# Kernel tuning notes

Hardware: AMD Instinct MI355X
Metric: run time of the kernel (lower is better)

Reference implementation:

```python
import math
import jax, jax.numpy as jnp
import numpy as np

L, B, N, D, H, DFF = 4, 64, 511, 256, 8, 512
S = N + 1          # +1 game token
HD = D // H
BW = 7             # BOARD_WIDTH (undefined global in source; board-game policy width)


def layer_norm(x, g, b):
    m = jnp.mean(x, axis=-1, keepdims=True)
    v = jnp.var(x, axis=-1, keepdims=True)
    return (x - m) / jnp.sqrt(v + 1e-5) * g + b


def setup_inputs() -> dict:
    key = jax.random.key(0)
    ks = jax.random.split(key, 24)

    def p(k, shape):
        return jax.random.normal(k, shape, jnp.float32) * 0.02

    return {
        "cell_states": jax.random.randint(ks[0], (B * N,), 0, 3, dtype=jnp.int32),
        "edge_type_matrix": jax.random.randint(ks[1], (B, N, N), 0, 3, dtype=jnp.int32),
        "patch_emb": p(ks[2], (3, D)),
        "game_token": p(ks[3], (1, 1, D)),
        "edge_emb": p(ks[4], (3, H)),   # zeros in source init; random here to exercise bias path
        "in_w": p(ks[5], (L, 3 * D, D)), "in_b": p(ks[6], (L, 3 * D)),
        "out_w": p(ks[7], (L, D, D)), "out_b": p(ks[8], (L, D)),
        "ff1_w": p(ks[9], (L, DFF, D)), "ff1_b": p(ks[10], (L, DFF)),
        "ff2_w": p(ks[11], (L, D, DFF)), "ff2_b": p(ks[12], (L, D)),
        "ln1_g": jnp.ones((L, D)), "ln1_b": jnp.zeros((L, D)),
        "ln2_g": jnp.ones((L, D)), "ln2_b": jnp.zeros((L, D)),
        "fc1_w": p(ks[13], (64, D)), "fc1_b": p(ks[14], (64,)),
        "pol_w": p(ks[15], (BW, 64)), "pol_b": p(ks[16], (BW,)),
        "val_w": p(ks[17], (1, 64)), "val_b": p(ks[18], (1,)),
    }


def reference(cell_states, edge_type_matrix, patch_emb, game_token, edge_emb,
              in_w, in_b, out_w, out_b, ff1_w, ff1_b, ff2_w, ff2_b,
              ln1_g, ln1_b, ln2_g, ln2_b, fc1_w, fc1_b, pol_w, pol_b, val_w, val_b):
    # embed cells and prepend game token -> [B, S, D]
    x = patch_emb[cell_states].reshape(B, N, D)
    x = jnp.concatenate([jnp.broadcast_to(game_token, (B, 1, D)), x], axis=1)

    # edge bias: [B,N,N,H] -> [B,H,N,N], pad token row/col with zeros -> [B,H,S,S]
    bias = jnp.transpose(edge_emb[edge_type_matrix], (0, 3, 1, 2))
    bias = jnp.pad(bias, ((0, 0), (0, 0), (1, 0), (1, 0)))

    scale = math.sqrt(HD)
    for i in range(L):
        h = layer_norm(x, ln1_g[i], ln1_b[i])
        qkv = h @ in_w[i].T + in_b[i]                       # [B,S,3D]
        q, k, v = jnp.split(qkv, 3, axis=-1)
        q = q.reshape(B, S, H, HD).transpose(0, 2, 1, 3)    # [B,H,S,HD]
        k = k.reshape(B, S, H, HD).transpose(0, 2, 1, 3)
        v = v.reshape(B, S, H, HD).transpose(0, 2, 1, 3)
        scores = jnp.einsum('bhqd,bhkd->bhqk', q, k) / scale + bias
        attn = jax.nn.softmax(scores, axis=-1)              # dropout = identity (eval)
        o = jnp.einsum('bhqk,bhkd->bhqd', attn, v)
        o = o.transpose(0, 2, 1, 3).reshape(B, S, D)
        x = x + (o @ out_w[i].T + out_b[i])
        h2 = layer_norm(x, ln2_g[i], ln2_b[i])
        x = x + (jax.nn.relu(h2 @ ff1_w[i].T + ff1_b[i]) @ ff2_w[i].T + ff2_b[i])

    g = x[:, 0, :]
    o = jax.nn.relu(g @ fc1_w.T + fc1_b)
    policy_logits = o @ pol_w.T + pol_b
    value = jnp.tanh(o @ val_w.T + val_b)
    return policy_logits, value
```

## Files before the change

### kernel.cpp

```cpp
#include <hip/hip_runtime.h>
#include <hip/hip_bf16.h>
#include <math.h>

#define L_ 4
#define B_ 64
#define N_ 511
#define D_ 256
#define H_ 8
#define DFF_ 512
#define S_ 512
#define HD_ 32
#define BW_ 7
#define BS_ (B_*S_)

typedef __attribute__((ext_vector_type(8))) short short8;
typedef __attribute__((ext_vector_type(4))) short short4v;
typedef __attribute__((ext_vector_type(4))) float f32x4;

#define L2E 1.44269504088896340f
#define QSCL (0.17677669529663687f * 1.44269504088896340f)

#if defined(__HIP_DEVICE_COMPILE__)
#if __has_builtin(__builtin_amdgcn_mfma_f32_16x16x16bf16_1k)
#define MFMA16(p, v, c) __builtin_amdgcn_mfma_f32_16x16x16bf16_1k(p, v, c, 0, 0, 0)
#elif __has_builtin(__builtin_amdgcn_mfma_f32_16x16x16_bf16)
#define MFMA16(p, v, c) __builtin_amdgcn_mfma_f32_16x16x16_bf16(p, v, c, 0, 0, 0)
#else
#define MFMA16(p, v, c) (c)
#endif
#else
#define MFMA16(p, v, c) (c)
#endif

#if defined(__HIP_DEVICE_COMPILE__) && __has_builtin(__builtin_amdgcn_exp2f)
#define EXP2(x) __builtin_amdgcn_exp2f(x)
#else
#define EXP2(x) exp2f(x)
#endif

__device__ inline ushort f2b(float f) {
    unsigned u = __float_as_uint(f);
    unsigned r = (u + 0x7fffu + ((u >> 16) & 1u)) >> 16;
    return (ushort)r;
}

#if defined(__HIP_DEVICE_COMPILE__) && __has_builtin(__builtin_amdgcn_cvt_pk_bf16_f32)
typedef __attribute__((ext_vector_type(2))) __bf16 bf16x2_t;
__device__ inline uint pk_bf16(float a, float b) {
    bf16x2_t r = __builtin_amdgcn_cvt_pk_bf16_f32(a, b);
    return *(uint*)&r;
}
#else
__device__ inline uint pk_bf16(float a, float b) {
    return (uint)f2b(a) | ((uint)f2b(b) << 16);
}
#endif

__device__ inline void bsel4(uint E, uint tlo, uint thi,
                             float b0, float b1, float b2, float bl[4]) {
#if defined(__HIP_DEVICE_COMPILE__) && __has_builtin(__builtin_amdgcn_perm)
    uint E2  = E + E;
    uint E2b = E2 | 0x01010101u;
    uint s01 = __builtin_amdgcn_perm(E2b, E2, 0x05010400u);
    uint s23 = __builtin_amdgcn_perm(E2b, E2, 0x07030602u);
    uint p01 = __builtin_amdgcn_perm(thi, tlo, s01);
    uint p23 = __builtin_amdgcn_perm(thi, tlo, s23);
    bl[0] = __uint_as_float(p01 << 16);
    bl[1] = __uint_as_float(p01 & 0xFFFF0000u);
    bl[2] = __uint_as_float(p23 << 16);
    bl[3] = __uint_as_float(p23 & 0xFFFF0000u);
#else
    #pragma unroll
    for (int i = 0; i < 4; i++) {
        unsigned char e = (unsigned char)((E >> (8 * i)) & 0xff);
        bl[i] = e == 0 ? b0 : (e == 1 ? b1 : (e == 2 ? b2 : 0.f));
    }
#endif
}

__device__ inline void gload16(const void* g, void* l) {
#if __has_builtin(__builtin_amdgcn_global_load_lds)
    __builtin_amdgcn_global_load_lds(
        (const __attribute__((address_space(1))) void*)g,
        (__attribute__((address_space(3))) void*)l, 16, 0, 0);
#else
    *(short8*)l = *(const short8*)g;
#endif
}

__global__ __launch_bounds__(256) void build_x(const int* __restrict__ cs,
                                               const float* __restrict__ patch,
                                               const float* __restrict__ game,
                                               float* __restrict__ x)
{
    int idx = blockIdx.x * 256 + threadIdx.x;
    int row = idx / (D_ / 4);
    int c4  = idx % (D_ / 4);
    int s = row & (S_ - 1);
    float4 v;
    if (s == 0) {
        v = ((const float4*)game)[c4];
    } else {
        int b = row / S_;
        int cell = cs[b * N_ + s - 1];
        v = ((const float4*)(patch + cell * D_))[c4];
    }
    ((float4*)x)[idx] = v;
}

__global__ __launch_bounds__(256) void build_et8(const int* __restrict__ et,
                                                 unsigned char* __restrict__ et8)
{
    long idx = (long)blockIdx.x * 256 + threadIdx.x;
    int k = (int)(idx & (S_ - 1));
    long rem = idx >> 9;
    int q = (int)(rem & (S_ - 1));
    int b = (int)(rem >> 9);
    unsigned char v = 3;
    if (q > 0 && k > 0) {
        v = (unsigned char)et[((long)b * N_ + (q - 1)) * N_ + (k - 1)];
    }
    et8[idx] = v;
}

__global__ __launch_bounds__(256) void convert_f2b(const float* __restrict__ in,
                                                   ushort* __restrict__ out, int n4)
{
    int i = blockIdx.x * 256 + threadIdx.x;
    if (i >= n4) return;
    float4 v = ((const float4*)in)[i];
    ushort4 o4;
    o4.x = f2b(v.x); o4.y = f2b(v.y); o4.z = f2b(v.z); o4.w = f2b(v.w);
    ((ushort4*)out)[i] = o4;
}

__global__ __launch_bounds__(256) void convert_inw(const float* __restrict__ in,
                                                   ushort* __restrict__ out)
{
    int i = blockIdx.x * 256 + threadIdx.x;
    if (i >= 196608) return;
    float4 v = ((const float4*)in)[i];
    int r = (i >> 6) % 768;
    float s = (r < 256) ? (float)QSCL : 1.f;
    ushort4 o4;
    o4.x = f2b(v.x * s); o4.y = f2b(v.y * s); o4.z = f2b(v.z * s); o4.w = f2b(v.w * s);
    ((ushort4*)out)[i] = o4;
}

__global__ __launch_bounds__(256) void ln_kernel(const float* __restrict__ in,
                                                 ushort* __restrict__ out,
                                                 const float* __restrict__ gw,
                                                 const float* __restrict__ bw)
{
    int t = threadIdx.x;
    int lane = t & 63;
    int r = t >> 6;
    size_t row = (size_t)blockIdx.x * 4 + r;
    float4 v = *(const float4*)(in + row * D_ + lane * 4);
    float s = v.x + v.y + v.z + v.w;
    #pragma unroll
    for (int o = 32; o >= 1; o >>= 1) s += __shfl_xor(s, o);
    float mean = s * (1.f / 256.f);
    float dx = v.x - mean, dy = v.y - mean, dz = v.z - mean, dw = v.w - mean;
    float s2 = dx * dx + dy * dy + dz * dz + dw * dw;
    #pragma unroll
    for (int o = 32; o >= 1; o >>= 1) s2 += __shfl_xor(s2, o);
    float rstd = rsqrtf(s2 * (1.f / 256.f) + 1e-5f);
    float4 g  = *(const float4*)(gw + lane * 4);
    float4 bb = *(const float4*)(bw + lane * 4);
    ushort4 o4;
    o4.x = f2b(dx * rstd * g.x + bb.x);
    o4.y = f2b(dy * rstd * g.y + bb.y);
    o4.z = f2b(dz * rstd * g.z + bb.z);
    o4.w = f2b(dw * rstd * g.w + bb.w);
    *(ushort4*)(out + row * D_ + lane * 4) = o4;
}

template<int K, int NT, bool RELU, bool QSC, bool QKV>
__global__ __launch_bounds__(256, 2) void gemm_lds(const ushort* __restrict__ A,
                                                   const ushort* __restrict__ W,
                                                   const float* __restrict__ bias,
                                                   ushort* __restrict__ Cout,
                                                   ushort* __restrict__ Kb,
                                                   ushort* __restrict__ Vt)
{
    __shared__ ushort As[4096];
    __shared__ ushort Ws[4096];
    const int N = NT * 128;
    int t = threadIdx.x;
    int wave = t >> 6, lane = t & 63;
    int lr = lane & 15, quad = lane >> 4;
    int lk = quad * 8;
    int blk = blockIdx.x;
    int xcd = blk & 7, idx = blk >> 3;
    int m0 = (xcd * 32 + (idx & 31)) * 128;
    int n0 = (idx >> 5) * 128;
    int mh = (wave >> 1) * 64, nh = (wave & 1) * 64;

    const ushort* ga0 = A + (size_t)(m0 + (t >> 2)) * K + (t & 3) * 8;
    const ushort* ga1 = ga0 + (size_t)64 * K;
    const ushort* gw0 = W + (size_t)(n0 + (t >> 2)) * K + (t & 3) * 8;
    const ushort* gw1 = gw0 + (size_t)64 * K;
    ushort* la0 = As + t * 8;
    ushort* la1 = As + t * 8 + 2048;
    ushort* lw0 = Ws + t * 8;
    ushort* lw1 = Ws + t * 8 + 2048;

    f32x4 acc[4][4];
    f32x4 zz = {0.f, 0.f, 0.f, 0.f};
    #pragma unroll
    for (int i = 0; i < 4; i++)
        #pragma unroll
        for (int j = 0; j < 4; j++) acc[i][j] = zz;

    for (int k0 = 0; k0 < K; k0 += 32) {
        gload16(ga0 + k0, la0);
        gload16(ga1 + k0, la1);
        gload16(gw0 + k0, lw0);
        gload16(gw1 + k0, lw1);
        __syncthreads();
        short8 af[4], wf[4];
        #pragma unroll
        for (int i = 0; i < 4; i++) af[i] = *(const short8*)&As[(mh + i * 16 + lr) * 32 + lk];
        #pragma unroll
        for (int j = 0; j < 4; j++) wf[j] = *(const short8*)&Ws[(nh + j * 16 + lr) * 32 + lk];
        #pragma unroll
        for (int i = 0; i < 4; i++)
            #pragma unroll
            for (int j = 0; j < 4; j++)
                acc[i][j] = __builtin_amdgcn_mfma_f32_16x16x32_bf16(af[i], wf[j], acc[i][j], 0, 0, 0);
        __syncthreads();
    }

    #pragma unroll
    for (int nt = 0; nt < 4; nt++) {
        int colbase = n0 + nh + nt * 16;
        int col = colbase + lr;
        float bv = bias[col];
        if (QSC && colbase < 256) bv *= (float)QSCL;
        int region = QKV ? (colbase >> 8) : 0;
        #pragma unroll
        for (int mt = 0; mt < 4; mt++) {
            int rowb = m0 + mh + mt * 16 + quad * 4;
            if (!QKV || region == 0) {
                #pragma unroll
                for (int r = 0; r < 4; r++) {
                    size_t cidx = (size_t)(rowb + r) * N + col;
                    float v = acc[mt][nt][r] + bv;
                    if (RELU) v = fmaxf(v, 0.f);
                    Cout[cidx] = f2b(v);
                }
            } else if (region == 1) {
                int hh = (col >> 5) & 7, d = col & 31;
                int bb = rowb >> 9, s = rowb & 511;
                size_t kbase = ((size_t)(bb * 8 + hh) * 512 + s) * 32 + d;
                #pragma unroll
                for (int r = 0; r < 4; r++)
                    Kb[kbase + (size_t)r * 32] = f2b(acc[mt][nt][r] + bv);
            } else {
                int hh = (col >> 5) & 7, d = col & 31;
                int bb = rowb >> 9, s = rowb & 511;
                ushort4 w;
                w.x = f2b(acc[mt][nt][0] + bv);
                w.y = f2b(acc[mt][nt][1] + bv);
                w.z = f2b(acc[mt][nt][2] + bv);
                w.w = f2b(acc[mt][nt][3] + bv);
                size_t vidx = (((size_t)(bb * 8 + hh) * 32 + (s >> 4)) * 32 + d) * 16 + (s & 15);
                *(ushort4*)&Vt[vidx] = w;
            }
        }
    }
}

template<int K>
__global__ __launch_bounds__(256, 2) void gemm_ln(const ushort* __restrict__ A,
                                                  const ushort* __restrict__ W,
                                                  const float* __restrict__ bias,
                                                  float* __restrict__ X,
                                                  const float* __restrict__ lng,
                                                  const float* __restrict__ lnb,
                                                  ushort* __restrict__ Hout)
{
    __shared__ ushort As[64 * 32];
    __shared__ ushort Ws[256 * 32];
    __shared__ float lds_s[64][4];
    __shared__ float lds_q[64][4];
    int t = threadIdx.x;
    int wave = t >> 6, lane = t & 63;
    int lr = lane & 15, quad = lane >> 4;
    int lk = quad * 8;
    int blk = blockIdx.x;
    int xcd = blk & 7;
    int m0 = (xcd * 64 + (blk >> 3)) * 64;
    int nh = wave * 64;

    const ushort* ga = A + (size_t)(m0 + (t >> 2)) * K + (t & 3) * 8;
    const ushort* gw = W + (size_t)(t >> 2) * K + (t & 3) * 8;
    ushort* la = As + t * 8;
    ushort* lw = Ws + t * 8;

    f32x4 acc[4][4];
    f32x4 zz = {0.f, 0.f, 0.f, 0.f};
    #pragma unroll
    for (int i = 0; i < 4; i++)
        #pragma unroll
        for (int j = 0; j < 4; j++) acc[i][j] = zz;

    for (int k0 = 0; k0 < K; k0 += 32) {
        gload16(ga + k0, la);
        #pragma unroll
        for (int j = 0; j < 4; j++)
            gload16(gw + (size_t)(j * 64) * K + k0, lw + j * 2048);
        __syncthreads();
        short8 af[4], wf[4];
        #pragma unroll
        for (int i = 0; i < 4; i++) af[i] = *(const short8*)&As[(i * 16 + lr) * 32 + lk];
        #pragma unroll
        for (int j = 0; j < 4; j++) wf[j] = *(const short8*)&Ws[(nh + j * 16 + lr) * 32 + lk];
        #pragma unroll
        for (int i = 0; i < 4; i++)
            #pragma unroll
            for (int j = 0; j < 4; j++)
                acc[i][j] = __builtin_amdgcn_mfma_f32_16x16x32_bf16(af[i], wf[j], acc[i][j], 0, 0, 0);
        __syncthreads();
    }

    float gc[4], bc[4], bi[4];
    #pragma unroll
    for (int nt = 0; nt < 4; nt++) {
        int col = nh + nt * 16 + lr;
        gc[nt] = lng[col]; bc[nt] = lnb[col]; bi[nt] = bias[col];
    }
    float psum[16], psq[16];
    #pragma unroll
    for (int e = 0; e < 16; e++) { psum[e] = 0.f; psq[e] = 0.f; }
    #pragma unroll
    for (int nt = 0; nt < 4; nt++) {
        #pragma unroll
        for (int mt = 0; mt < 4; mt++) {
            #pragma unroll
            for (int r = 0; r < 4; r++) {
                int row = m0 + mt * 16 + quad * 4 + r;
                size_t idx = (size_t)row * D_ + nh + nt * 16 + lr;
                float v = acc[mt][nt][r] + bi[nt] + X[idx];
                X[idx] = v;
                acc[mt][nt][r] = v;
                psum[mt * 4 + r] += v;
                psq[mt * 4 + r]  += v * v;
            }
        }
    }
    #pragma unroll
    for (int e = 0; e < 16; e++) {
        float s = psum[e], q = psq[e];
        s += __shfl_xor(s, 1); q += __shfl_xor(q, 1);
        s += __shfl_xor(s, 2); q += __shfl_xor(q, 2);
        s += __shfl_xor(s, 4); q += __shfl_xor(q, 4);
        s += __shfl_xor(s, 8); q += __shfl_xor(q, 8);
        psum[e] = s; psq[e] = q;
    }
    if (lr == 0) {
        #pragma unroll
        for (int mt = 0; mt < 4; mt++)
            #pragma unroll
            for (int r = 0; r < 4; r++) {
                int rl = mt * 16 + quad * 4 + r;
                lds_s[rl][wave] = psum[mt * 4 + r];
                lds_q[rl][wave] = psq[mt * 4 + r];
            }
    }
    __syncthreads();
    #pragma unroll
    for (int mt = 0; mt < 4; mt++) {
        #pragma unroll
        for (int r = 0; r < 4; r++) {
            int rl = mt * 16 + quad * 4 + r;
            f32x4 ss = *(const f32x4*)lds_s[rl];
            f32x4 qq = *(const f32x4*)lds_q[rl];
            float s = ss[0] + ss[1] + ss[2] + ss[3];
            float q = qq[0] + qq[1] + qq[2] + qq[3];
            float mean = s * (1.f / 256.f);
            float rstd = rsqrtf(q * (1.f / 256.f) - mean * mean + 1e-5f);
            int row = m0 + mt * 16 + quad * 4 + r;
            #pragma unroll
            for (int nt = 0; nt < 4; nt++) {
                size_t idx = (size_t)row * D_ + nh + nt * 16 + lr;
                float hv = (acc[mt][nt][r] - mean) * rstd * gc[nt] + bc[nt];
                Hout[idx] = f2b(hv);
            }
        }
    }
}

__global__ __launch_bounds__(256, 4) void attn_mfma(const ushort* __restrict__ qkv,
                                                    const ushort* __restrict__ Kb,
                                                    const ushort* __restrict__ Vt,
                                                    const unsigned char* __restrict__ et8,
                                                    const float* __restrict__ eemb,
                                                    ushort* __restrict__ o)
{
    __shared__ unsigned char Est[2][2][4096];
    int t = threadIdx.x;
    int wave = t >> 6, lane = t & 63;
    int lr = lane & 15, quad = lane >> 4;
    int lk = quad * 8;
    int blk = blockIdx.x;
    int b = ((blk >> 7) << 3) | (blk & 7);
    int rest = (blk >> 3) & 15;
    int h = rest & 7;
    int qhalf = rest >> 3;
    int bh = b * 8 + h;
    int q0 = qhalf * 256 + wave * 64;
    float eb0 = eemb[h] * L2E, eb1 = eemb[8 + h] * L2E, eb2 = eemb[16 + h] * L2E;
    uint tlo = (uint)f2b(eb0) | ((uint)f2b(eb1) << 16);
    uint thi = (uint)f2b(eb2);

    short8 qf[4];
    #pragma unroll
    for (int X = 0; X < 4; X++)
        qf[X] = *(const short8*)(qkv + ((size_t)(b * S_ + q0 + X * 16 + lr)) * 768 + h * 32 + lk);
    const ushort* Kp = Kb + ((size_t)(bh * S_ + lr)) * 32 + lk;
    const ushort* Vp = Vt + (size_t)bh * 32 * 512 + lr * 16 + quad * 4;
    const unsigned char* Ep = et8 + ((size_t)(b * S_ + qhalf * 256 + t)) * S_;
    unsigned char* ElD = &Est[0][0][t * 16];

    f32x4 zz = {0.f, 0.f, 0.f, 0.f};
    f32x4 oacc[4][2];
    float lsum[4];
    #pragma unroll
    for (int X = 0; X < 4; X++) { oacc[X][0] = zz; oacc[X][1] = zz; lsum[X] = 0.f; }

    gload16(Ep + 0,  ElD);
    gload16(Ep + 16, ElD + 4096);
    short8 kf0 = *(const short8*)(Kp);
    short8 kf1 = *(const short8*)(Kp + 16 * 32);
    __syncthreads();

    for (int k0 = 0; k0 < S_; k0 += 32) {
        int cb = (k0 >> 5) & 1, nb = cb ^ 1;
        if (k0 < S_ - 32) {
            gload16(Ep + k0 + 32, ElD + (size_t)nb * 8192);
            gload16(Ep + k0 + 48, ElD + (size_t)nb * 8192 + 4096);
        }
        int kn = (k0 + 32) & (S_ - 1);
        short8 nk0 = *(const short8*)(Kp + (size_t)kn * 32);
        short8 nk1 = *(const short8*)(Kp + (size_t)(kn + 16) * 32);
        const ushort* vt0 = Vp + (size_t)(k0 >> 4) * 512;
        short4v vf00 = *(const short4v*)(vt0);
        short4v vf01 = *(const short4v*)(vt0 + 256);
        short4v vf10 = *(const short4v*)(vt0 + 512);
        short4v vf11 = *(const short4v*)(vt0 + 768);
        #pragma unroll
        for (int X = 0; X < 4; X++) {
            f32x4 s0 = __builtin_amdgcn_mfma_f32_16x16x32_bf16(kf0, qf[X], zz, 0, 0, 0);
            f32x4 s1 = __builtin_amdgcn_mfma_f32_16x16x32_bf16(kf1, qf[X], zz, 0, 0, 0);
            int qrow = wave * 64 + X * 16 + lr;
            uint E0 = *(const uint*)&Est[cb][0][qrow * 16 + quad * 4];
            uint E1 = *(const uint*)&Est[cb][1][qrow * 16 + quad * 4];
            float bl0[4], bl1[4];
            bsel4(E0, tlo, thi, eb0, eb1, eb2, bl0);
            bsel4(E1, tlo, thi, eb0, eb1, eb2, bl1);
            float p0[4], p1[4];
            #pragma unroll
            for (int r = 0; r < 4; r++) {
                p0[r] = EXP2(s0[r] + bl0[r]);
                p1[r] = EXP2(s1[r] + bl1[r]);
                lsum[X] += p0[r] + p1[r];
            }
            union { short4v v; uint2 u; } P0, P1;
            P0.u.x = pk_bf16(p0[0], p0[1]); P0.u.y = pk_bf16(p0[2], p0[3]);
            P1.u.x = pk_bf16(p1[0], p1[1]); P1.u.y = pk_bf16(p1[2], p1[3]);
            oacc[X][0] = MFMA16(P0.v, vf00, oacc[X][0]);
            oacc[X][1] = MFMA16(P0.v, vf01, oacc[X][1]);
            oacc[X][0] = MFMA16(P1.v, vf10, oacc[X][0]);
            oacc[X][1] = MFMA16(P1.v, vf11, oacc[X][1]);
        }
        kf0 = nk0; kf1 = nk1;
        __syncthreads();
    }

    #pragma unroll
    for (int X = 0; X < 4; X++) {
        float ls = lsum[X];
        ls += __shfl_xor(ls, 16);
        ls += __shfl_xor(ls, 32);
        #pragma unroll
        for (int r = 0; r < 4; r++) {
            int q = quad * 4 + r;
            float inv = 1.f / __shfl(ls, q);
            size_t base = (size_t)(b * S_ + q0 + X * 16 + q) * D_ + h * 32;
            o[base + lr]      = f2b(oacc[X][0][r] * inv);
            o[base + 16 + lr] = f2b(oacc[X][1][r] * inv);
        }
    }
}

__global__ __launch_bounds__(64) void head_kernel(const float* __restrict__ x,
                                                  const float* __restrict__ fc1w,
                                                  const float* __restrict__ fc1b,
                                                  const float* __restrict__ polw,
                                                  const float* __restrict__ polb,
                                                  const float* __restrict__ valw,
                                                  const float* __restrict__ valb,
                                                  float* __restrict__ out)
{
    __shared__ float o1[64];
    int b = blockIdx.x;
    int t = threadIdx.x;
    const float* g = x + (size_t)b * S_ * D_;
    float acc = fc1b[t];
    for (int k = 0; k < D_; k++) acc += g[k] * fc1w[t * D_ + k];
    o1[t] = fmaxf(acc, 0.f);
    __syncthreads();
    if (t < BW_) {
        float a = polb[t];
        for (int k = 0; k < 64; k++) a += o1[k] * polw[t * 64 + k];
        out[b * BW_ + t] = a;
    } else if (t == BW_) {
        float a = valb[0];
        for (int k = 0; k < 64; k++) a += o1[k] * valw[k];
        out[B_ * BW_ + b] = tanhf(a);
    }
}

extern "C" void kernel_launch(void* const* d_in, const int* in_sizes, int n_in,
                              void* d_out, int out_size, void* d_ws, size_t ws_size,
                              hipStream_t stream)
{
    const int*   cs    = (const int*)d_in[0];
    const int*   etm   = (const int*)d_in[1];
    const float* patch = (const float*)d_in[2];
    const float* game  = (const float*)d_in[3];
    const float* eemb  = (const float*)d_in[4];
    const float* in_w  = (const float*)d_in[5];
    const float* in_b  = (const float*)d_in[6];
    const float* out_w = (const float*)d_in[7];
    const float* out_b = (const float*)d_in[8];
    const float* ff1_w = (const float*)d_in[9];
    const float* ff1_b = (const float*)d_in[10];
    const float* ff2_w = (const float*)d_in[11];
    const float* ff2_b = (const float*)d_in[12];
    const float* ln1_g = (const float*)d_in[13];
    const float* ln1_b = (const float*)d_in[14];
    const float* ln2_g = (const float*)d_in[15];
    const float* ln2_b = (const float*)d_in[16];
    const float* fc1_w = (const float*)d_in[17];
    const float* fc1_b = (const float*)d_in[18];
    const float* pol_w = (const float*)d_in[19];
    const float* pol_b = (const float*)d_in[20];
    const float* val_w = (const float*)d_in[21];
    const float* val_b = (const float*)d_in[22];
    float* out = (float*)d_out;

    char* base = (char*)d_ws;
    float*  x     = (float*)(base + 0);
    ushort* h     = (ushort*)(base + 33554432);
    ushort* qkvb  = (ushort*)(base + 50331648);
    ushort* Kb    = (ushort*)(base + 100663296);
    ushort* Vt    = (ushort*)(base + 117440512);
    ushort* ob    = (ushort*)(base + 134217728);
    unsigned char* et8 = (unsigned char*)(base + 150994944);
    ushort* inwb  = (ushort*)(base + 167772160);
    ushort* outwb = (ushort*)(base + 169345024);
    ushort* ff1wb = (ushort*)(base + 169869312);
    ushort* ff2wb = (ushort*)(base + 170917888);

    build_x<<<8192, 256, 0, stream>>>(cs, patch, game, x);
    build_et8<<<65536, 256, 0, stream>>>(etm, et8);
    convert_inw<<<768, 256, 0, stream>>>(in_w, inwb);
    convert_f2b<<<256, 256, 0, stream>>>(out_w, outwb, 65536);
    convert_f2b<<<512, 256, 0, stream>>>(ff1_w, ff1wb, 131072);
    convert_f2b<<<512, 256, 0, stream>>>(ff2_w, ff2wb, 131072);

    ln_kernel<<<8192, 256, 0, stream>>>(x, h, ln1_g, ln1_b);

    for (int i = 0; i < L_; i++) {
        gemm_lds<256, 6, false, true, true><<<1536, 256, 0, stream>>>(
            h, inwb + (size_t)i * 196608, in_b + i * 768, qkvb, Kb, Vt);
        attn_mfma<<<1024, 256, 0, stream>>>(qkvb, Kb, Vt, et8, eemb, ob);
        gemm_ln<256><<<512, 256, 0, stream>>>(
            ob, outwb + (size_t)i * 65536, out_b + i * 256, x,
            ln2_g + i * D_, ln2_b + i * D_, h);
        gemm_lds<256, 4, true, false, false><<<1024, 256, 0, stream>>>(
            h, ff1wb + (size_t)i * 131072, ff1_b + i * 512, qkvb, nullptr, nullptr);
        int nx = (i + 1 < L_) ? (i + 1) : i;
        gemm_ln<512><<<512, 256, 0, stream>>>(
            qkvb, ff2wb + (size_t)i * 131072, ff2_b + i * 256, x,
            ln1_g + nx * D_, ln1_b + nx * D_, h);
    }
    head_kernel<<<B_, 64, 0, stream>>>(x, fc1_w, fc1_b, pol_w, pol_b, val_w, val_b, out);
}
```

Before: 797.3 us.

## Split attention into quarter-query blocks, fold bias into MFMA, compute row sums via MFMA

```diff
diff --git a/kernel.cpp b/kernel.cpp
--- a/kernel.cpp
+++ b/kernel.cpp
@@ -56,8 +56,8 @@
 }
 #endif
 
-__device__ inline void bsel4(uint E, uint tlo, uint thi,
-                             float b0, float b1, float b2, float bl[4]) {
+__device__ inline f32x4 bsel4v(uint E, uint tlo, uint thi) {
+    f32x4 r;
 #if defined(__HIP_DEVICE_COMPILE__) && __has_builtin(__builtin_amdgcn_perm)
     uint E2  = E + E;
     uint E2b = E2 | 0x01010101u;
@@ -65,17 +65,20 @@
     uint s23 = __builtin_amdgcn_perm(E2b, E2, 0x07030602u);
     uint p01 = __builtin_amdgcn_perm(thi, tlo, s01);
     uint p23 = __builtin_amdgcn_perm(thi, tlo, s23);
-    bl[0] = __uint_as_float(p01 << 16);
-    bl[1] = __uint_as_float(p01 & 0xFFFF0000u);
-    bl[2] = __uint_as_float(p23 << 16);
-    bl[3] = __uint_as_float(p23 & 0xFFFF0000u);
+    r[0] = __uint_as_float(p01 << 16);
+    r[1] = __uint_as_float(p01 & 0xFFFF0000u);
+    r[2] = __uint_as_float(p23 << 16);
+    r[3] = __uint_as_float(p23 & 0xFFFF0000u);
 #else
     #pragma unroll
     for (int i = 0; i < 4; i++) {
         unsigned char e = (unsigned char)((E >> (8 * i)) & 0xff);
-        bl[i] = e == 0 ? b0 : (e == 1 ? b1 : (e == 2 ? b2 : 0.f));
+        uint bb = e == 0 ? (tlo & 0xFFFFu) : (e == 1 ? (tlo >> 16) :
+                  (e == 2 ? (thi & 0xFFFFu) : 0u));
+        r[i] = __uint_as_float(bb << 16);
     }
 #endif
+    return r;
 }
 
 __device__ inline void gload16(const void* g, void* l) {
@@ -392,46 +395,47 @@
     }
 }
 
-__global__ __launch_bounds__(256, 4) void attn_mfma(const ushort* __restrict__ qkv,
+__global__ __launch_bounds__(256, 8) void attn_mfma(const ushort* __restrict__ qkv,
                                                     const ushort* __restrict__ Kb,
                                                     const ushort* __restrict__ Vt,
                                                     const unsigned char* __restrict__ et8,
                                                     const float* __restrict__ eemb,
                                                     ushort* __restrict__ o)
 {
-    __shared__ unsigned char Est[2][2][4096];
+    __shared__ unsigned char Est[2][2][2048];
     int t = threadIdx.x;
     int wave = t >> 6, lane = t & 63;
     int lr = lane & 15, quad = lane >> 4;
     int lk = quad * 8;
     int blk = blockIdx.x;
-    int b = ((blk >> 7) << 3) | (blk & 7);
-    int rest = (blk >> 3) & 15;
-    int h = rest & 7;
-    int qhalf = rest >> 3;
+    int b = ((blk >> 8) << 3) | (blk & 7);
+    int h = (blk >> 3) & 7;
+    int qq = (blk >> 6) & 3;
     int bh = b * 8 + h;
-    int q0 = qhalf * 256 + wave * 64;
+    int q0 = qq * 128 + wave * 32;
     float eb0 = eemb[h] * L2E, eb1 = eemb[8 + h] * L2E, eb2 = eemb[16 + h] * L2E;
     uint tlo = (uint)f2b(eb0) | ((uint)f2b(eb1) << 16);
     uint thi = (uint)f2b(eb2);
 
-    short8 qf[4];
-    #pragma unroll
-    for (int X = 0; X < 4; X++)
+    short8 qf[2];
+    #pragma unroll
+    for (int X = 0; X < 2; X++)
         qf[X] = *(const short8*)(qkv + ((size_t)(b * S_ + q0 + X * 16 + lr)) * 768 + h * 32 + lk);
     const ushort* Kp = Kb + ((size_t)(bh * S_ + lr)) * 32 + lk;
     const ushort* Vp = Vt + (size_t)bh * 32 * 512 + lr * 16 + quad * 4;
-    const unsigned char* Ep = et8 + ((size_t)(b * S_ + qhalf * 256 + t)) * S_;
-    unsigned char* ElD = &Est[0][0][t * 16];
+    int ehalf = wave >> 1;
+    int erow = ((wave & 1) << 6) | lane;
+    const unsigned char* Ep = et8 + ((size_t)(b * S_ + qq * 128 + erow)) * S_ + ehalf * 16;
+    unsigned char* ElD = &Est[0][ehalf][erow * 16];
+
+    const short4v vones = { (short)0x3F80, (short)0x3F80, (short)0x3F80, (short)0x3F80 };
 
     f32x4 zz = {0.f, 0.f, 0.f, 0.f};
-    f32x4 oacc[4][2];
-    float lsum[4];
-    #pragma unroll
-    for (int X = 0; X < 4; X++) { oacc[X][0] = zz; oacc[X][1] = zz; lsum[X] = 0.f; }
-
-    gload16(Ep + 0,  ElD);
-    gload16(Ep + 16, ElD + 4096);
+    f32x4 oacc[2][2], lacc[2];
+    #pragma unroll
+    for (int X = 0; X < 2; X++) { oacc[X][0] = zz; oacc[X][1] = zz; lacc[X] = zz; }
+
+    gload16(Ep, ElD);
     short8 kf0 = *(const short8*)(Kp);
     short8 kf1 = *(const short8*)(Kp + 16 * 32);
     __syncthreads();
@@ -439,8 +443,7 @@
     for (int k0 = 0; k0 < S_; k0 += 32) {
         int cb = (k0 >> 5) & 1, nb = cb ^ 1;
         if (k0 < S_ - 32) {
-            gload16(Ep + k0 + 32, ElD + (size_t)nb * 8192);
-            gload16(Ep + k0 + 48, ElD + (size_t)nb * 8192 + 4096);
+            gload16(Ep + k0 + 32, ElD + (size_t)nb * 4096);
         }
         int kn = (k0 + 32) & (S_ - 1);
         short8 nk0 = *(const short8*)(Kp + (size_t)kn * 32);
@@ -451,43 +454,40 @@
         short4v vf10 = *(const short4v*)(vt0 + 512);
         short4v vf11 = *(const short4v*)(vt0 + 768);
         #pragma unroll
-        for (int X = 0; X < 4; X++) {
-            f32x4 s0 = __builtin_amdgcn_mfma_f32_16x16x32_bf16(kf0, qf[X], zz, 0, 0, 0);
-            f32x4 s1 = __builtin_amdgcn_mfma_f32_16x16x32_bf16(kf1, qf[X], zz, 0, 0, 0);
-            int qrow = wave * 64 + X * 16 + lr;
+        for (int X = 0; X < 2; X++) {
+            int qrow = wave * 32 + X * 16 + lr;
             uint E0 = *(const uint*)&Est[cb][0][qrow * 16 + quad * 4];
             uint E1 = *(const uint*)&Est[cb][1][qrow * 16 + quad * 4];
-            float bl0[4], bl1[4];
-            bsel4(E0, tlo, thi, eb0, eb1, eb2, bl0);
-            bsel4(E1, tlo, thi, eb0, eb1, eb2, bl1);
+            f32x4 c0 = bsel4v(E0, tlo, thi);
+            f32x4 c1 = bsel4v(E1, tlo, thi);
+            f32x4 s0 = __builtin_amdgcn_mfma_f32_16x16x32_bf16(kf0, qf[X], c0, 0, 0, 0);
+            f32x4 s1 = __builtin_amdgcn_mfma_f32_16x16x32_bf16(kf1, qf[X], c1, 0, 0, 0);
             float p0[4], p1[4];
             #pragma unroll
             for (int r = 0; r < 4; r++) {
-                p0[r] = EXP2(s0[r] + bl0[r]);
-                p1[r] = EXP2(s1[r] + bl1[r]);
-                lsum[X] += p0[r] + p1[r];
+                p0[r] = EXP2(s0[r]);
+                p1[r] = EXP2(s1[r]);
             }
             union { short4v v; uint2 u; } P0, P1;
             P0.u.x = pk_bf16(p0[0], p0[1]); P0.u.y = pk_bf16(p0[2], p0[3]);
             P1.u.x = pk_bf16(p1[0], p1[1]); P1.u.y = pk_bf16(p1[2], p1[3]);
             oacc[X][0] = MFMA16(P0.v, vf00, oacc[X][0]);
             oacc[X][1] = MFMA16(P0.v, vf01, oacc[X][1]);
+            lacc[X]    = MFMA16(P0.v, vones, lacc[X]);
             oacc[X][0] = MFMA16(P1.v, vf10, oacc[X][0]);
             oacc[X][1] = MFMA16(P1.v, vf11, oacc[X][1]);
+            lacc[X]    = MFMA16(P1.v, vones, lacc[X]);
         }
         kf0 = nk0; kf1 = nk1;
         __syncthreads();
     }
 
     #pragma unroll
-    for (int X = 0; X < 4; X++) {
-        float ls = lsum[X];
-        ls += __shfl_xor(ls, 16);
-        ls += __shfl_xor(ls, 32);
+    for (int X = 0; X < 2; X++) {
         #pragma unroll
         for (int r = 0; r < 4; r++) {
             int q = quad * 4 + r;
-            float inv = 1.f / __shfl(ls, q);
+            float inv = 1.f / lacc[X][r];
             size_t base = (size_t)(b * S_ + q0 + X * 16 + q) * D_ + h * 32;
             o[base + lr]      = f2b(oacc[X][0][r] * inv);
             o[base + 16 + lr] = f2b(oacc[X][1][r] * inv);
@@ -577,7 +577,7 @@
     for (int i = 0; i < L_; i++) {
         gemm_lds<256, 6, false, true, true><<<1536, 256, 0, stream>>>(
             h, inwb + (size_t)i * 196608, in_b + i * 768, qkvb, Kb, Vt);
-        attn_mfma<<<1024, 256, 0, stream>>>(qkvb, Kb, Vt, et8, eemb, ob);
+        attn_mfma<<<2048, 256, 0, stream>>>(qkvb, Kb, Vt, et8, eemb, ob);
         gemm_ln<256><<<512, 256, 0, stream>>>(
             ob, outwb + (size_t)i * 65536, out_b + i * 256, x,
             ln2_g + i * D_, ln2_b + i * D_, h);
```

Measured after the change: 801.7 us. About the same (+0.5%).
